# Kernel tuning notes

Measured on AMD Instinct MI355X. Metric: run time of the kernel, lower is better.

The kernel has to match this reference:

```python
import jax, jax.numpy as jnp
import numpy as np

N = 256    # num_nodes = 2*K*R
K = 16     # num_cluster (after reflection pairing)
R = 8      # ratio = size of each original cluster
IN = 32
OUT = 32
BS = 32


def setup_inputs() -> dict:
    key = jax.random.key(0)
    k1, k2, k3, k4 = jax.random.split(key, 4)
    x = jax.random.normal(k1, (BS, N, IN), dtype=jnp.float32)
    w_diag = jax.random.uniform(k2, (IN * OUT, K), dtype=jnp.float32)           # torch.rand
    w_off = jax.random.uniform(k3, (IN * OUT, K, 2 * K), dtype=jnp.float32)     # torch.rand
    stdv = 1.0 / np.sqrt(OUT)
    b1 = jax.random.uniform(k4, (OUT,), minval=-stdv, maxval=stdv, dtype=jnp.float32)
    perm = np.random.default_rng(0).permutation(N)   # flatten_ids of shuffled clusters
    permute_ids = jnp.asarray(perm, dtype=jnp.int32)
    inv_permute = jnp.asarray(np.argsort(perm), dtype=jnp.int32)
    return {"x": x, "w_diag": w_diag, "w_off": w_off, "b1": b1,
            "permute_ids": permute_ids, "inv_permute": inv_permute}


def _build_W(w_diag, w_off):
    # Faithful to: kron(tie_weights(w_off), ones(R,R))/N + kron(diag_embed(repeat_interleave(w_diag,2)), eye(R))
    C = w_diag.shape[0]            # in*out channels
    width = 2 * K
    # tie_weights: interleave original rows with pair-swapped-column rows
    swap = np.arange(width).reshape(-1, 2)[:, ::-1].reshape(-1)      # [1,0,3,2,...]
    tied = jnp.stack([w_off, w_off[:, :, swap]], axis=2).reshape(C, width, width)
    # kron with ones(R,R) == repeat each entry R times along both node axes
    W3 = jnp.repeat(jnp.repeat(tied, R, axis=1), R, axis=2) / N      # (C, N, N)
    # kron(diag_embed(.), eye(R)) == add per-node diagonal, constant within cluster
    wd_full = jnp.repeat(jnp.repeat(w_diag, 2, axis=1), R, axis=1)   # (C, N)
    di = jnp.arange(N)
    W3 = W3.at[:, di, di].add(wd_full)
    # rearrange '(o i) j k -> (o j) (i k)'
    return W3.reshape(OUT, IN, N, N).transpose(0, 2, 1, 3).reshape(OUT * N, IN * N)


def reference(x, w_diag, w_off, b1, permute_ids, inv_permute):
    W = _build_W(w_diag, w_off)                       # (OUT*N, IN*N)
    xp = x[:, permute_ids, :]                         # (BS, N, IN) permuted
    xp = xp.transpose(0, 2, 1).reshape(BS, IN * N)    # feature-major flatten
    out = xp @ W.T                                    # (BS, OUT*N)
    out = out.reshape(BS, OUT, N).transpose(0, 2, 1)  # (BS, N, OUT)
    out = out[:, inv_permute, :] + b1[None, None, :]
    return out
```

## Files before the change

kernel.cpp:

```cpp
#include <hip/hip_runtime.h>

#define N_   256
#define IN_  32
#define OUT_ 32
#define BS_  32

__global__ __launch_bounds__(256) void k_prep(const float* __restrict__ x,
                                              const int* __restrict__ perm,
                                              const float* __restrict__ w_diag,
                                              float* __restrict__ ws_y,
                                              float* __restrict__ ws_wdT) {
    const int t = threadIdx.x;
    const int s = blockIdx.x;
    __shared__ int perm_s[256];
    perm_s[t] = perm[t];
    __syncthreads();
    const float* xs = x + s * (N_ * IN_);
#pragma unroll
    for (int k = 0; k < 4; ++k) {
        const int idx = k * 256 + t;
        const int q = idx >> 5;
        const int i = idx & 31;
        float sum = 0.f;
#pragma unroll
        for (int j = 0; j < 8; ++j)
            sum += xs[perm_s[8 * q + j] * IN_ + i];
        ws_y[(s * 32 + q) * 32 + i] = sum;
    }
    if (s == 0) {
#pragma unroll
        for (int m = 0; m < 64; ++m) {
            const int idx = m * 256 + t;
            const int c = idx >> 4;
            const int u = idx & 15;
            ws_wdT[u * 1024 + c] = w_diag[idx];
        }
    }
}

__global__ __launch_bounds__(256) void k_z(const float* __restrict__ w_off,
                                           const float* __restrict__ ws_y,
                                           float* __restrict__ ws_z) {
    const int t = threadIdx.x;
    const int b = blockIdx.x;
    const int o  = b & 31;
    const int sg = b >> 5;
    const int u  = t & 15;
    const int i4 = (t >> 4) & 7;
    const int sh = t >> 7;

    __shared__ float y_lds[4 * 32 * 32];
    __shared__ float part[128][8];

    {
        const float4* ysrc = (const float4*)(ws_y + sg * 4096);
        float4* ydst = (float4*)y_lds;
#pragma unroll
        for (int k = 0; k < 4; ++k)
            ydst[k * 256 + t] = ysrc[k * 256 + t];
    }

    float4 wv[4][8];
    const float* wbase = w_off + ((o * 32 + i4 * 4) * 16 + u) * 32;
#pragma unroll
    for (int di = 0; di < 4; ++di)
#pragma unroll
        for (int q4 = 0; q4 < 8; ++q4)
            wv[di][q4] = *(const float4*)(wbase + di * 512 + q4 * 4);

    __syncthreads();

#define WEL(di, qq) (((const float*)&wv[di][(qq) >> 2])[(qq) & 3])

    float accs[2][2];
#pragma unroll
    for (int dsi = 0; dsi < 2; ++dsi) {
        const float* yb = y_lds + (sh * 2 + dsi) * 1024 + i4 * 4;
        float a0 = 0.f, a1 = 0.f;
#pragma unroll
        for (int q = 0; q < 32; ++q) {
            const float4 yv = *(const float4*)(yb + q * 32);
            const int q1 = q ^ 1;
            a0 += WEL(0, q)  * yv.x + WEL(1, q)  * yv.y + WEL(2, q)  * yv.z + WEL(3, q)  * yv.w;
            a1 += WEL(0, q1) * yv.x + WEL(1, q1) * yv.y + WEL(2, q1) * yv.z + WEL(3, q1) * yv.w;
        }
        accs[dsi][0] = a0;
        accs[dsi][1] = a1;
    }
#undef WEL

#pragma unroll
    for (int dsi = 0; dsi < 2; ++dsi)
#pragma unroll
        for (int p = 0; p < 2; ++p) {
            const int slot = ((sh * 2 + dsi) * 16 + u) * 2 + p;
            part[slot][i4] = accs[dsi][p];
        }
    __syncthreads();

    if (t < 128) {
        float sum = 0.f;
#pragma unroll
        for (int j = 0; j < 8; ++j) sum += part[t][j];
        const int s_local = t >> 5;
        const int uu = (t >> 1) & 15;
        const int pp = t & 1;
        const int s = sg * 4 + s_local;
        ws_z[((s * 32 + o) * 16 + uu) * 2 + pp] = sum * (1.0f / 256.0f);
    }
}

__global__ __launch_bounds__(256) void k_out(const float* __restrict__ x,
                                             const int* __restrict__ perm,
                                             const float* __restrict__ b1,
                                             const float* __restrict__ ws_z,
                                             const float* __restrict__ ws_wdT,
                                             float* __restrict__ out) {
    const int t = threadIdx.x;
    const int b = blockIdx.x;
    const int s = b >> 3;
    const int ac = b & 7;

    __shared__ float xrow[32 * 32];
    __shared__ float wdt[2][32 * 36];
    __shared__ float z_lds[1024];
    __shared__ int perm_lds[32];

    if (t < 32) perm_lds[t] = perm[ac * 32 + t];

    ((float4*)z_lds)[t] = ((const float4*)(ws_z + s * 1024))[t];

    {
        const int o = t >> 3;
        const int ii = (t & 7) * 4;
#pragma unroll
        for (int uu = 0; uu < 2; ++uu) {
            const float4 v = *(const float4*)(ws_wdT + (ac * 2 + uu) * 1024 + o * 32 + ii);
            *(float4*)&wdt[uu][o * 36 + ii] = v;
        }
    }
    {
        const int r = t >> 3;
        const int col = (t & 7) * 4;
        const int rowp = perm[ac * 32 + r];
        const float4 v = *(const float4*)(x + (s * N_ + rowp) * IN_ + col);
        *(float4*)&xrow[r * 32 + col] = v;
    }
    __syncthreads();

    const int o = t & 31;
    const int rg = t >> 5;
    const int u_sel = rg >> 2;
    const int p = (rg >> 1) & 1;
    const int u = ac * 2 + u_sel;

    float4 wreg[8];
#pragma unroll
    for (int ii = 0; ii < 8; ++ii)
        wreg[ii] = *(const float4*)&wdt[u_sel][o * 36 + ii * 4];

    const float base = b1[o] + z_lds[(o * 16 + u) * 2 + p];

#pragma unroll
    for (int dr = 0; dr < 4; ++dr) {
        const int r = rg * 4 + dr;
        const float4* xr = (const float4*)&xrow[r * 32];
        float acc = base;
#pragma unroll
        for (int ii = 0; ii < 8; ++ii) {
            const float4 xv = xr[ii];
            const float4 wv = wreg[ii];
            acc += xv.x * wv.x + xv.y * wv.y + xv.z * wv.z + xv.w * wv.w;
        }
        out[(s * N_ + perm_lds[r]) * OUT_ + o] = acc;
    }
}

extern "C" void kernel_launch(void* const* d_in, const int* in_sizes, int n_in,
                              void* d_out, int out_size, void* d_ws, size_t ws_size,
                              hipStream_t stream) {
    const float* x      = (const float*)d_in[0];
    const float* w_diag = (const float*)d_in[1];
    const float* w_off  = (const float*)d_in[2];
    const float* b1     = (const float*)d_in[3];
    const int*   perm   = (const int*)d_in[4];

    float* out = (float*)d_out;
    float* ws = (float*)d_ws;
    float* ws_y   = ws;
    float* ws_z   = ws + 32768;
    float* ws_wdT = ws + 65536;

    k_prep<<<32, 256, 0, stream>>>(x, perm, w_diag, ws_y, ws_wdT);
    k_z<<<256, 256, 0, stream>>>(w_off, ws_y, ws_z);
    k_out<<<256, 256, 0, stream>>>(x, perm, b1, ws_z, ws_wdT, out);
}
```

Measured before the change: 83.88 us.

## Fuse cluster-sum prep into z kernel and read w_diag directly in output kernel

Removes the separate prep kernel: each z block now recomputes the permuted cluster sums of x for its 4 samples straight into shared memory. The output kernel gathers w_diag with strided scalar loads instead of reading a pre-transposed workspace copy. This saves one launch and the global round trip through the workspace. In exchange, every one of the 32 o-blocks per sample group redoes the same cluster-sum gather, and the w_diag loads are now uncoalesced.

Result: faster. 75.51 us, median of 2 (-10.0%).

```diff
diff --git a/kernel.cpp b/kernel.cpp
--- a/kernel.cpp
+++ b/kernel.cpp
@@ -5,42 +5,10 @@
 #define OUT_ 32
 #define BS_  32
 
-__global__ __launch_bounds__(256) void k_prep(const float* __restrict__ x,
-                                              const int* __restrict__ perm,
-                                              const float* __restrict__ w_diag,
-                                              float* __restrict__ ws_y,
-                                              float* __restrict__ ws_wdT) {
-    const int t = threadIdx.x;
-    const int s = blockIdx.x;
-    __shared__ int perm_s[256];
-    perm_s[t] = perm[t];
-    __syncthreads();
-    const float* xs = x + s * (N_ * IN_);
-#pragma unroll
-    for (int k = 0; k < 4; ++k) {
-        const int idx = k * 256 + t;
-        const int q = idx >> 5;
-        const int i = idx & 31;
-        float sum = 0.f;
-#pragma unroll
-        for (int j = 0; j < 8; ++j)
-            sum += xs[perm_s[8 * q + j] * IN_ + i];
-        ws_y[(s * 32 + q) * 32 + i] = sum;
-    }
-    if (s == 0) {
-#pragma unroll
-        for (int m = 0; m < 64; ++m) {
-            const int idx = m * 256 + t;
-            const int c = idx >> 4;
-            const int u = idx & 15;
-            ws_wdT[u * 1024 + c] = w_diag[idx];
-        }
-    }
-}
-
-__global__ __launch_bounds__(256) void k_z(const float* __restrict__ w_off,
-                                           const float* __restrict__ ws_y,
-                                           float* __restrict__ ws_z) {
+__global__ __launch_bounds__(256) void k_yz(const float* __restrict__ x,
+                                            const int* __restrict__ perm,
+                                            const float* __restrict__ w_off,
+                                            float* __restrict__ ws_z) {
     const int t = threadIdx.x;
     const int b = blockIdx.x;
     const int o  = b & 31;
@@ -49,16 +17,11 @@
     const int i4 = (t >> 4) & 7;
     const int sh = t >> 7;
 
+    __shared__ int   perm_s[256];
     __shared__ float y_lds[4 * 32 * 32];
     __shared__ float part[128][8];
 
-    {
-        const float4* ysrc = (const float4*)(ws_y + sg * 4096);
-        float4* ydst = (float4*)y_lds;
-#pragma unroll
-        for (int k = 0; k < 4; ++k)
-            ydst[k * 256 + t] = ysrc[k * 256 + t];
-    }
+    perm_s[t] = perm[t];
 
     float4 wv[4][8];
     const float* wbase = w_off + ((o * 32 + i4 * 4) * 16 + u) * 32;
@@ -68,6 +31,25 @@
         for (int q4 = 0; q4 < 8; ++q4)
             wv[di][q4] = *(const float4*)(wbase + di * 512 + q4 * 4);
 
+    __syncthreads();
+
+    {
+        const int i  = t & 31;
+        const int qb = t >> 5;
+#pragma unroll
+        for (int sl = 0; sl < 4; ++sl) {
+            const float* xs = x + (sg * 4 + sl) * (N_ * IN_);
+#pragma unroll
+            for (int k = 0; k < 4; ++k) {
+                const int q = qb * 4 + k;
+                float sum = 0.f;
+#pragma unroll
+                for (int j = 0; j < 8; ++j)
+                    sum += xs[perm_s[8 * q + j] * IN_ + i];
+                y_lds[sl * 1024 + q * 32 + i] = sum;
+            }
+        }
+    }
     __syncthreads();
 
 #define WEL(di, qq) (((const float*)&wv[di][(qq) >> 2])[(qq) & 3])
@@ -112,9 +94,9 @@
 
 __global__ __launch_bounds__(256) void k_out(const float* __restrict__ x,
                                              const int* __restrict__ perm,
+                                             const float* __restrict__ w_diag,
                                              const float* __restrict__ b1,
                                              const float* __restrict__ ws_z,
-                                             const float* __restrict__ ws_wdT,
                                              float* __restrict__ out) {
     const int t = threadIdx.x;
     const int b = blockIdx.x;
@@ -134,10 +116,10 @@
         const int o = t >> 3;
         const int ii = (t & 7) * 4;
 #pragma unroll
-        for (int uu = 0; uu < 2; ++uu) {
-            const float4 v = *(const float4*)(ws_wdT + (ac * 2 + uu) * 1024 + o * 32 + ii);
-            *(float4*)&wdt[uu][o * 36 + ii] = v;
-        }
+        for (int uu = 0; uu < 2; ++uu)
+#pragma unroll
+            for (int d = 0; d < 4; ++d)
+                wdt[uu][o * 36 + ii + d] = w_diag[(o * 32 + ii + d) * 16 + ac * 2 + uu];
     }
     {
         const int r = t >> 3;
@@ -186,12 +168,8 @@
     const int*   perm   = (const int*)d_in[4];
 
     float* out = (float*)d_out;
-    float* ws = (float*)d_ws;
-    float* ws_y   = ws;
-    float* ws_z   = ws + 32768;
-    float* ws_wdT = ws + 65536;
+    float* ws_z = (float*)d_ws;
 
-    k_prep<<<32, 256, 0, stream>>>(x, perm, w_diag, ws_y, ws_wdT);
-    k_z<<<256, 256, 0, stream>>>(w_off, ws_y, ws_z);
-    k_out<<<256, 256, 0, stream>>>(x, perm, b1, ws_z, ws_wdT, out);
+    k_yz<<<256, 256, 0, stream>>>(x, perm, w_off, ws_z);
+    k_out<<<256, 256, 0, stream>>>(x, perm, w_diag, b1, ws_z, out);
 }
```
